# Kernel optimization log

Hardware: AMD Instinct MI355X
Metric: run time of the kernel (lower is better)

The kernel has to match this reference:

```python
import jax, jax.numpy as jnp
import numpy as np

DIM = 96
HEADS = 3
HEAD_DIM = 32
MLP_DIM = 384
WS = 4  # window size (cubic)


def _rel_indices(ws):
    # relative position indices for a ws^3 window, offset to [0, 2*ws-2]
    coords = np.stack(np.meshgrid(np.arange(ws), np.arange(ws), np.arange(ws), indexing='ij'), -1).reshape(-1, 3)
    rel = coords[:, None, :] - coords[None, :, :] + (ws - 1)  # (n, n, 3)
    return jnp.asarray(rel, dtype=jnp.int32)


def _layer_norm(x, g, b, eps=1e-5):
    m = x.mean(-1, keepdims=True)
    v = x.var(-1, keepdims=True)
    return (x - m) * jax.lax.rsqrt(v + eps) * g + b


def setup_inputs() -> dict:
    key = jax.random.key(0)
    ks = jax.random.split(key, 12)
    inner = HEADS * HEAD_DIM
    s = lambda fan_in: 1.0 / np.sqrt(fan_in)
    return {
        'x': jax.random.normal(ks[0], (2, 128, 128, 8, DIM), dtype=jnp.float32),
        'ln1_g': jnp.ones((DIM,), jnp.float32),
        'ln1_b': jnp.zeros((DIM,), jnp.float32),
        'w_qkv': jax.random.normal(ks[1], (DIM, 3 * inner), jnp.float32) * s(DIM),
        'w_out': jax.random.normal(ks[2], (inner, DIM), jnp.float32) * s(inner),
        'b_out': jnp.zeros((DIM,), jnp.float32),
        'pos_tab': jax.random.normal(ks[3], (2 * WS - 1, 2 * WS - 1, 2 * WS - 1), jnp.float32),
        'ln2_g': jnp.ones((DIM,), jnp.float32),
        'ln2_b': jnp.zeros((DIM,), jnp.float32),
        'w1': jax.random.normal(ks[4], (DIM, MLP_DIM), jnp.float32) * s(DIM),
        'b1': jnp.zeros((MLP_DIM,), jnp.float32),
        'w2': jax.random.normal(ks[5], (MLP_DIM, DIM), jnp.float32) * s(MLP_DIM),
        'b2': jnp.zeros((DIM,), jnp.float32),
    }


def reference(x, ln1_g, ln1_b, w_qkv, w_out, b_out, pos_tab, ln2_g, ln2_b, w1, b1, w2, b2):
    B, H, W, D, C = x.shape
    h, d, ws = HEADS, HEAD_DIM, WS
    nH, nW, nD = H // ws, W // ws, D // ws
    n = ws ** 3
    scale = d ** -0.5

    # --- window attention block (PreNorm + Residual) ---
    y = _layer_norm(x, ln1_g, ln1_b)
    qkv = y @ w_qkv  # (B,H,W,D,3*h*d)
    qkv = qkv.reshape(B, nH, ws, nW, ws, nD, ws, 3, h, d)
    qkv = qkv.transpose(7, 0, 8, 1, 3, 5, 2, 4, 6, 9)  # (3,B,h,nH,nW,nD,ws,ws,ws,d)
    qkv = qkv.reshape(3, B, h, nH * nW * nD, n, d)
    q, k, v = qkv[0], qkv[1], qkv[2]

    attn = jnp.einsum('bhwid,bhwjd->bhwij', q, k) * scale  # (B,h,nw,n,n)
    rel = _rel_indices(ws)
    bias = pos_tab[rel[..., 0], rel[..., 1], rel[..., 2]]  # (n,n)
    attn = jax.nn.softmax(attn + bias, axis=-1)
    o = jnp.einsum('bhwij,bhwjd->bhwid', attn, v)  # (B,h,nw,n,d)

    o = o.reshape(B, h, nH, nW, nD, ws, ws, ws, d)
    o = o.transpose(0, 2, 5, 3, 6, 4, 7, 1, 8).reshape(B, H, W, D, h * d)
    x = x + (o @ w_out + b_out)

    # --- MLP block (PreNorm + Residual), GELU exact to match nn.GELU ---
    y = _layer_norm(x, ln2_g, ln2_b)
    y = jax.nn.gelu(y @ w1 + b1, approximate=False) @ w2 + b2
    return x + y
```

## Files before the change

### kernel.cpp

```cpp
#include <hip/hip_runtime.h>

#define DIM 96
#define HEADS 3
#define HD 32
#define MLPD 384
#define NTOK 64
#define YP 104
#define QKP 200
#define VP 72
#define WSP 104
#define HP 40
#define W1P 104
#define W2P 40
#define X1P 100
#define W2PF 36
#define CH 32
#define NCH 12
#define WQT_OFF 147456
#define WOT_OFF 175104
#define WS2_NEEDED 368640

typedef unsigned short ushort_t;
typedef unsigned int uint_t;
typedef __attribute__((ext_vector_type(8))) short bf16x8;
typedef __attribute__((ext_vector_type(4))) float f32x4;

__device__ inline float b2f(ushort_t u) {
    return __uint_as_float(((uint_t)u) << 16);
}
__device__ inline ushort_t f2b(float f) {
    uint_t u = __float_as_uint(f);
    uint_t r = u + 0x7FFFu + ((u >> 16) & 1u);
    return (ushort_t)(r >> 16);
}
__device__ inline void split2(float v, ushort_t& hi, ushort_t& lo) {
    hi = f2b(v);
    float d = v - b2f(hi);
    lo = f2b(d);
}
__device__ inline void split_pack2(float v0, float v1, uint_t& hi2, uint_t& lo2) {
    uint_t u0 = __float_as_uint(v0), u1 = __float_as_uint(v1);
    hi2 = __builtin_amdgcn_perm(u1, u0, 0x07060302u);
    float d0 = v0 - __uint_as_float(u0 & 0xFFFF0000u);
    float d1 = v1 - __uint_as_float(u1 & 0xFFFF0000u);
    lo2 = __builtin_amdgcn_perm(__float_as_uint(d1), __float_as_uint(d0), 0x07060302u);
}
__device__ inline size_t grow(int bb, int wh, int ww, int wd, int t) {
    return ((size_t)((bb * 128 + wh * 4 + (t >> 4)) * 128 + ww * 4 + ((t >> 2) & 3)) * 8
            + wd * 4 + (t & 3));
}
__device__ inline float gelu_fast(float v) {
    float z = v * 0.70710678118654752f;
    float az = fabsf(z);
    float k = __frcp_rn(1.0f + 0.3275911f * az);
    float poly = k * (0.254829592f + k * (-0.284496736f + k * (1.421413741f
                 + k * (-1.453152027f + k * 1.061405429f))));
    float e = 1.0f - poly * __expf(-az * az);
    float erfv = copysignf(e, z);
    return 0.5f * v * (1.0f + erfv);
}

__global__ __launch_bounds__(256) void prep_weights(
    const float* __restrict__ w1, const float* __restrict__ w2,
    const float* __restrict__ w_qkv, const float* __restrict__ w_out,
    ushort_t* __restrict__ wt)
{
    int idx = blockIdx.x * 256 + threadIdx.x;
    if (idx >= 96 * MLPD) return;
    {
        int k = idx / MLPD, col = idx % MLPD;
        ushort_t h, l;
        split2(w1[idx], h, l);
        wt[col * 96 + k] = h;
        wt[36864 + col * 96 + k] = l;
    }
    {
        int k = idx / 96, n = idx % 96;
        int c = k >> 5, f = k & 31;
        int p = ((f & 15) >> 2) * 8 + (f >> 4) * 4 + (f & 3);
        ushort_t h, l;
        split2(w2[idx], h, l);
        wt[73728  + n * MLPD + c * 32 + p] = h;
        wt[110592 + n * MLPD + c * 32 + p] = l;
    }
    if (idx < 288 * 96) {
        int f = idx / 96, k = idx % 96;
        wt[WQT_OFF + f * 96 + k] = f2b(w_qkv[k * 288 + f]);
    }
    if (idx < 96 * 96) {
        int n = idx / 96, k = idx % 96;
        wt[WOT_OFF + n * 96 + k] = f2b(w_out[k * 96 + n]);
    }
}

__global__ __launch_bounds__(256, 3) void swin_fused_kernel(
    const float* __restrict__ x,
    const float* __restrict__ ln1_g, const float* __restrict__ ln1_b,
    const ushort_t* __restrict__ wt,
    const float* __restrict__ b_out, const float* __restrict__ pos_tab,
    const float* __restrict__ ln2_g, const float* __restrict__ ln2_b,
    const float* __restrict__ b1v, const float* __restrict__ b2v,
    float* __restrict__ out)
{
    __shared__ ushort_t ybuf[NTOK * YP];
    __shared__ ushort_t qkbuf[NTOK * QKP];
    __shared__ ushort_t vbuf[96 * VP];

    const ushort_t* wqkvt = wt + WQT_OFF;
    const ushort_t* woutt = wt + WOT_OFF;
    float* x1f = reinterpret_cast<float*>(qkbuf);

    const int tid = threadIdx.x;
    const int wv = tid >> 6;
    const int lane = tid & 63;
    const int lr = lane & 15;
    const int lk = lane >> 4;

    const int wid = blockIdx.x;
    const int wd = wid & 1;
    const int ww = (wid >> 1) & 31;
    const int wh = (wid >> 6) & 31;
    const int bb = wid >> 11;

    float breg[4][4];
    {
        const int cb = lr >> 2, cc = lr & 3;
        #pragma unroll
        for (int nt = 0; nt < 4; ++nt)
            #pragma unroll
            for (int r = 0; r < 4; ++r)
                breg[nt][r] = pos_tab[((wv - nt + 3) * 7 + (lk - cb + 3)) * 7 + (r - cc + 3)];
    }

    {
        const int t = tid >> 2, part = tid & 3;
        const float* xr = x + grow(bb, wh, ww, wd, t) * DIM + part * 24;
        float vals[24];
        #pragma unroll
        for (int i = 0; i < 6; ++i) {
            float4 v4 = *reinterpret_cast<const float4*>(xr + i * 4);
            vals[i * 4 + 0] = v4.x; vals[i * 4 + 1] = v4.y;
            vals[i * 4 + 2] = v4.z; vals[i * 4 + 3] = v4.w;
        }
        float s = 0.f, sq = 0.f;
        #pragma unroll
        for (int i = 0; i < 24; ++i) { s += vals[i]; sq += vals[i] * vals[i]; }
        s  += __shfl_xor(s, 1);  s  += __shfl_xor(s, 2);
        sq += __shfl_xor(sq, 1); sq += __shfl_xor(sq, 2);
        float mean = s * (1.f / 96.f);
        float var  = sq * (1.f / 96.f) - mean * mean;
        float rstd = rsqrtf(var + 1e-5f);
        #pragma unroll
        for (int i = 0; i < 24; i += 2) {
            int c = part * 24 + i;
            float v0 = (vals[i]     - mean) * rstd * ln1_g[c]     + ln1_b[c];
            float v1 = (vals[i + 1] - mean) * rstd * ln1_g[c + 1] + ln1_b[c + 1];
            *reinterpret_cast<uint_t*>(&ybuf[t * YP + c]) =
                (uint_t)f2b(v0) | ((uint_t)f2b(v1) << 16);
        }
    }
    asm volatile("s_waitcnt lgkmcnt(0)" ::: "memory");

    bf16x8 ay[3];
    #pragma unroll
    for (int ks = 0; ks < 3; ++ks)
        ay[ks] = *reinterpret_cast<const bf16x8*>(&ybuf[(wv * 16 + lr) * YP + ks * 32 + lk * 8]);

    #pragma unroll 3
    for (int ch = 0; ch < 9; ++ch) {
        #pragma unroll
        for (int nt = 0; nt < 2; ++nt) {
            const int feat = ch * 32 + nt * 16 + lr;
            const ushort_t* wb = &wqkvt[feat * 96 + lk * 8];
            bf16x8 b0 = *reinterpret_cast<const bf16x8*>(wb);
            bf16x8 b1 = *reinterpret_cast<const bf16x8*>(wb + 32);
            bf16x8 b2 = *reinterpret_cast<const bf16x8*>(wb + 64);
            f32x4 acc = (f32x4){0.f, 0.f, 0.f, 0.f};
            acc = __builtin_amdgcn_mfma_f32_16x16x32_bf16(ay[0], b0, acc, 0, 0, 0);
            acc = __builtin_amdgcn_mfma_f32_16x16x32_bf16(ay[1], b1, acc, 0, 0, 0);
            acc = __builtin_amdgcn_mfma_f32_16x16x32_bf16(ay[2], b2, acc, 0, 0, 0);
            if (ch < 6) {
                #pragma unroll
                for (int r = 0; r < 4; ++r)
                    qkbuf[(wv * 16 + lk * 4 + r) * QKP + feat] = f2b(acc[r]);
            } else {
                #pragma unroll
                for (int r = 0; r < 4; ++r)
                    vbuf[(feat - 192) * VP + wv * 16 + lk * 4 + r] = f2b(acc[r]);
            }
        }
    }
    __syncthreads();

    const float scale = 0.17677669529663687f;
    f32x4 oacc[6];
    #pragma unroll
    for (int i = 0; i < 6; ++i) oacc[i] = (f32x4){0.f, 0.f, 0.f, 0.f};
    ushort_t* pb = &ybuf[wv * 16 * VP];

    for (int h = 0; h < HEADS; ++h) {
        bf16x8 aq = *reinterpret_cast<const bf16x8*>(&qkbuf[(wv * 16 + lr) * QKP + h * HD + lk * 8]);
        float s[4][4];
        #pragma unroll
        for (int nt = 0; nt < 4; ++nt) {
            bf16x8 bk = *reinterpret_cast<const bf16x8*>(&qkbuf[(nt * 16 + lr) * QKP + 96 + h * HD + lk * 8]);
            f32x4 acc = (f32x4){0.f, 0.f, 0.f, 0.f};
            acc = __builtin_amdgcn_mfma_f32_16x16x32_bf16(aq, bk, acc, 0, 0, 0);
            #pragma unroll
            for (int r = 0; r < 4; ++r) s[nt][r] = acc[r] * scale + breg[nt][r];
        }
        float m[4], sum[4], inv[4];
        #pragma unroll
        for (int r = 0; r < 4; ++r) {
            m[r] = fmaxf(fmaxf(s[0][r], s[1][r]), fmaxf(s[2][r], s[3][r]));
            for (int mk = 1; mk < 16; mk <<= 1) m[r] = fmaxf(m[r], __shfl_xor(m[r], mk));
        }
        #pragma unroll
        for (int r = 0; r < 4; ++r) sum[r] = 0.f;
        #pragma unroll
        for (int nt = 0; nt < 4; ++nt)
            #pragma unroll
            for (int r = 0; r < 4; ++r) { s[nt][r] = __expf(s[nt][r] - m[r]); sum[r] += s[nt][r]; }
        #pragma unroll
        for (int r = 0; r < 4; ++r) {
            for (int mk = 1; mk < 16; mk <<= 1) sum[r] += __shfl_xor(sum[r], mk);
            inv[r] = 1.f / sum[r];
        }
        #pragma unroll
        for (int nt = 0; nt < 4; ++nt)
            #pragma unroll
            for (int r = 0; r < 4; ++r)
                pb[(lk * 4 + r) * VP + nt * 16 + lr] = f2b(s[nt][r] * inv[r]);
        asm volatile("s_waitcnt lgkmcnt(0)" ::: "memory");

        bf16x8 pa0 = *reinterpret_cast<const bf16x8*>(&pb[lr * VP + 0 * 32 + lk * 8]);
        bf16x8 pa1 = *reinterpret_cast<const bf16x8*>(&pb[lr * VP + 1 * 32 + lk * 8]);
        #pragma unroll
        for (int nt2 = 0; nt2 < 2; ++nt2) {
            f32x4 acc = oacc[h * 2 + nt2];
            bf16x8 bv0 = *reinterpret_cast<const bf16x8*>(&vbuf[(h * HD + nt2 * 16 + lr) * VP + 0 * 32 + lk * 8]);
            bf16x8 bv1 = *reinterpret_cast<const bf16x8*>(&vbuf[(h * HD + nt2 * 16 + lr) * VP + 1 * 32 + lk * 8]);
            acc = __builtin_amdgcn_mfma_f32_16x16x32_bf16(pa0, bv0, acc, 0, 0, 0);
            acc = __builtin_amdgcn_mfma_f32_16x16x32_bf16(pa1, bv1, acc, 0, 0, 0);
            oacc[h * 2 + nt2] = acc;
        }
    }
    __syncthreads();

    #pragma unroll
    for (int nt = 0; nt < 6; ++nt)
        #pragma unroll
        for (int r = 0; r < 4; ++r)
            ybuf[(wv * 16 + lk * 4 + r) * YP + nt * 16 + lr] = f2b(oacc[nt][r]);
    asm volatile("s_waitcnt lgkmcnt(0)" ::: "memory");

    bf16x8 ao[3];
    #pragma unroll
    for (int ks = 0; ks < 3; ++ks)
        ao[ks] = *reinterpret_cast<const bf16x8*>(&ybuf[(wv * 16 + lr) * YP + ks * 32 + lk * 8]);
    #pragma unroll
    for (int nt = 0; nt < 6; ++nt) {
        const ushort_t* wb = &woutt[(nt * 16 + lr) * 96 + lk * 8];
        f32x4 acc = (f32x4){0.f, 0.f, 0.f, 0.f};
        acc = __builtin_amdgcn_mfma_f32_16x16x32_bf16(ao[0], *reinterpret_cast<const bf16x8*>(wb), acc, 0, 0, 0);
        acc = __builtin_amdgcn_mfma_f32_16x16x32_bf16(ao[1], *reinterpret_cast<const bf16x8*>(wb + 32), acc, 0, 0, 0);
        acc = __builtin_amdgcn_mfma_f32_16x16x32_bf16(ao[2], *reinterpret_cast<const bf16x8*>(wb + 64), acc, 0, 0, 0);
        int col = nt * 16 + lr;
        float bias = b_out[col];
        #pragma unroll
        for (int r = 0; r < 4; ++r) {
            int t = wv * 16 + lk * 4 + r;
            x1f[t * X1P + col] = acc[r] + bias + x[grow(bb, wh, ww, wd, t) * DIM + col];
        }
    }
    asm volatile("s_waitcnt lgkmcnt(0)" ::: "memory");

    const ushort_t* gb[6];
    ushort_t* lp[6];
    #pragma unroll
    for (int i = 0; i < 6; ++i) {
        int o = tid + i * 256;
        if (i < 3) {
            int p = o / 384, rem = o % 384, r = rem / 12, j = rem % 12;
            gb[i] = wt + p * 36864 + r * 96 + j * 8;
            lp[i] = &ybuf[p * 3328 + r * 104 + j * 8];
        } else {
            int q = o - 768;
            int p = q / 384, rem = q % 384, n = rem / 4, j = rem % 4;
            gb[i] = wt + 73728 + p * 36864 + n * 384 + j * 8;
            lp[i] = &vbuf[p * 3456 + n * W2PF + j * 8];
        }
    }
    bf16x8 pf[6];
    #pragma unroll
    for (int i = 0; i < 6; ++i)
        pf[i] = *reinterpret_cast<const bf16x8*>(gb[i]);

    bf16x8 ah[3], al[3];
    {
        const int row = wv * 16 + lr;
        float v[3][8];
        float s = 0.f, sq = 0.f;
        #pragma unroll
        for (int ks = 0; ks < 3; ++ks) {
            float4 a4 = *reinterpret_cast<const float4*>(&x1f[row * X1P + ks * 32 + lk * 8]);
            float4 b4 = *reinterpret_cast<const float4*>(&x1f[row * X1P + ks * 32 + lk * 8 + 4]);
            v[ks][0] = a4.x; v[ks][1] = a4.y; v[ks][2] = a4.z; v[ks][3] = a4.w;
            v[ks][4] = b4.x; v[ks][5] = b4.y; v[ks][6] = b4.z; v[ks][7] = b4.w;
            #pragma unroll
            for (int j = 0; j < 8; ++j) { s += v[ks][j]; sq += v[ks][j] * v[ks][j]; }
        }
        s  += __shfl_xor(s, 16);  s  += __shfl_xor(s, 32);
        sq += __shfl_xor(sq, 16); sq += __shfl_xor(sq, 32);
        float mean = s * (1.f / 96.f);
        float var  = sq * (1.f / 96.f) - mean * mean;
        float rstd = rsqrtf(var + 1e-5f);
        #pragma unroll
        for (int ks = 0; ks < 3; ++ks) {
            float4 g4a = *reinterpret_cast<const float4*>(&ln2_g[ks * 32 + lk * 8]);
            float4 g4b = *reinterpret_cast<const float4*>(&ln2_g[ks * 32 + lk * 8 + 4]);
            float4 b4a = *reinterpret_cast<const float4*>(&ln2_b[ks * 32 + lk * 8]);
            float4 b4b = *reinterpret_cast<const float4*>(&ln2_b[ks * 32 + lk * 8 + 4]);
            float g[8] = {g4a.x, g4a.y, g4a.z, g4a.w, g4b.x, g4b.y, g4b.z, g4b.w};
            float bbv[8] = {b4a.x, b4a.y, b4a.z, b4a.w, b4b.x, b4b.y, b4b.z, b4b.w};
            float y[8];
            #pragma unroll
            for (int j = 0; j < 8; ++j)
                y[j] = (v[ks][j] - mean) * rstd * g[j] + bbv[j];
            union { uint4 u; bf16x8 f; } H, L;
            split_pack2(y[0], y[1], H.u.x, L.u.x);
            split_pack2(y[2], y[3], H.u.y, L.u.y);
            split_pack2(y[4], y[5], H.u.z, L.u.z);
            split_pack2(y[6], y[7], H.u.w, L.u.w);
            ah[ks] = H.f;
            al[ks] = L.f;
        }
    }

    f32x4 macc[6];
    #pragma unroll
    for (int nt = 0; nt < 6; ++nt) macc[nt] = (f32x4){0.f, 0.f, 0.f, 0.f};

    for (int c = 0; c < NCH; ++c) {
        __syncthreads();
        #pragma unroll
        for (int i = 0; i < 6; ++i)
            *reinterpret_cast<bf16x8*>(lp[i]) = pf[i];
        if (c + 1 < NCH) {
            const int coff1 = (c + 1) * 3072, coff2 = (c + 1) * 32;
            #pragma unroll
            for (int i = 0; i < 3; ++i)
                pf[i] = *reinterpret_cast<const bf16x8*>(gb[i] + coff1);
            #pragma unroll
            for (int i = 3; i < 6; ++i)
                pf[i] = *reinterpret_cast<const bf16x8*>(gb[i] + coff2);
        }
        __syncthreads();

        f32x4 hpre[2];
        #pragma unroll
        for (int nt = 0; nt < 2; ++nt) {
            const int roff = (nt * 16 + lr) * 104 + lk * 8;
            bf16x8 wh0 = *reinterpret_cast<const bf16x8*>(&ybuf[roff]);
            bf16x8 wh1 = *reinterpret_cast<const bf16x8*>(&ybuf[roff + 32]);
            bf16x8 wh2 = *reinterpret_cast<const bf16x8*>(&ybuf[roff + 64]);
            bf16x8 wl0 = *reinterpret_cast<const bf16x8*>(&ybuf[3328 + roff]);
            bf16x8 wl1 = *reinterpret_cast<const bf16x8*>(&ybuf[3328 + roff + 32]);
            bf16x8 wl2 = *reinterpret_cast<const bf16x8*>(&ybuf[3328 + roff + 64]);
            f32x4 acc = (f32x4){0.f, 0.f, 0.f, 0.f};
            acc = __builtin_amdgcn_mfma_f32_16x16x32_bf16(wh0, ah[0], acc, 0, 0, 0);
            acc = __builtin_amdgcn_mfma_f32_16x16x32_bf16(wh0, al[0], acc, 0, 0, 0);
            acc = __builtin_amdgcn_mfma_f32_16x16x32_bf16(wl0, ah[0], acc, 0, 0, 0);
            acc = __builtin_amdgcn_mfma_f32_16x16x32_bf16(wh1, ah[1], acc, 0, 0, 0);
            acc = __builtin_amdgcn_mfma_f32_16x16x32_bf16(wh1, al[1], acc, 0, 0, 0);
            acc = __builtin_amdgcn_mfma_f32_16x16x32_bf16(wl1, ah[1], acc, 0, 0, 0);
            acc = __builtin_amdgcn_mfma_f32_16x16x32_bf16(wh2, ah[2], acc, 0, 0, 0);
            acc = __builtin_amdgcn_mfma_f32_16x16x32_bf16(wh2, al[2], acc, 0, 0, 0);
            acc = __builtin_amdgcn_mfma_f32_16x16x32_bf16(wl2, ah[2], acc, 0, 0, 0);
            hpre[nt] = acc;
        }

        float4 b40 = *reinterpret_cast<const float4*>(&b1v[c * CH + 0 * 16 + lk * 4]);
        float4 b41 = *reinterpret_cast<const float4*>(&b1v[c * CH + 1 * 16 + lk * 4]);
        bf16x8 a2h, a2l;
        {
            float g0 = gelu_fast(hpre[0][0] + b40.x);
            float g1 = gelu_fast(hpre[0][1] + b40.y);
            float g2 = gelu_fast(hpre[0][2] + b40.z);
            float g3 = gelu_fast(hpre[0][3] + b40.w);
            float g4 = gelu_fast(hpre[1][0] + b41.x);
            float g5 = gelu_fast(hpre[1][1] + b41.y);
            float g6 = gelu_fast(hpre[1][2] + b41.z);
            float g7 = gelu_fast(hpre[1][3] + b41.w);
            union { uint4 u; bf16x8 f; } H, L;
            split_pack2(g0, g1, H.u.x, L.u.x);
            split_pack2(g2, g3, H.u.y, L.u.y);
            split_pack2(g4, g5, H.u.z, L.u.z);
            split_pack2(g6, g7, H.u.w, L.u.w);
            a2h = H.f;
            a2l = L.f;
        }

        #pragma unroll
        for (int nt2 = 0; nt2 < 6; ++nt2) {
            const int noff = (nt2 * 16 + lr) * W2PF + lk * 8;
            bf16x8 wh = *reinterpret_cast<const bf16x8*>(&vbuf[noff]);
            bf16x8 wl = *reinterpret_cast<const bf16x8*>(&vbuf[3456 + noff]);
            f32x4 acc = macc[nt2];
            acc = __builtin_amdgcn_mfma_f32_16x16x32_bf16(a2h, wh, acc, 0, 0, 0);
            acc = __builtin_amdgcn_mfma_f32_16x16x32_bf16(a2h, wl, acc, 0, 0, 0);
            acc = __builtin_amdgcn_mfma_f32_16x16x32_bf16(a2l, wh, acc, 0, 0, 0);
            macc[nt2] = acc;
        }
    }

    #pragma unroll
    for (int nt = 0; nt < 6; ++nt) {
        int col = nt * 16 + lr;
        float bias = b2v[col];
        #pragma unroll
        for (int r = 0; r < 4; ++r) {
            int t = wv * 16 + lk * 4 + r;
            out[grow(bb, wh, ww, wd, t) * DIM + col] =
                macc[nt][r] + bias + x1f[t * X1P + col];
        }
    }
}

__global__ __launch_bounds__(256) void attn_mfma_kernel(
    const float* __restrict__ x,
    const float* __restrict__ ln1_g, const float* __restrict__ ln1_b,
    const float* __restrict__ w_qkv,
    const float* __restrict__ w_out, const float* __restrict__ b_out,
    const float* __restrict__ pos_tab,
    float* __restrict__ out)
{
    __shared__ ushort_t ybuf[NTOK * YP];
    __shared__ ushort_t qkbuf[NTOK * QKP];
    __shared__ ushort_t vbuf[96 * VP];
    __shared__ ushort_t wstage[CH * WSP];
    __shared__ float pos[343];

    const int tid = threadIdx.x;
    const int wv = tid >> 6;
    const int lane = tid & 63;
    const int lr = lane & 15;
    const int lk = lane >> 4;

    const int wid = blockIdx.x;
    const int wd = wid & 1;
    const int ww = (wid >> 1) & 31;
    const int wh = (wid >> 6) & 31;
    const int bb = wid >> 11;

    for (int e = tid; e < 343; e += 256) pos[e] = pos_tab[e];

    {
        const int t = tid >> 2, part = tid & 3;
        const float* xr = x + grow(bb, wh, ww, wd, t) * DIM + part * 24;
        float vals[24];
        for (int i = 0; i < 6; ++i) {
            float4 v4 = *reinterpret_cast<const float4*>(xr + i * 4);
            vals[i * 4 + 0] = v4.x; vals[i * 4 + 1] = v4.y;
            vals[i * 4 + 2] = v4.z; vals[i * 4 + 3] = v4.w;
        }
        float s = 0.f, sq = 0.f;
        for (int i = 0; i < 24; ++i) { s += vals[i]; sq += vals[i] * vals[i]; }
        s  += __shfl_xor(s, 1);  s  += __shfl_xor(s, 2);
        sq += __shfl_xor(sq, 1); sq += __shfl_xor(sq, 2);
        float mean = s * (1.f / 96.f);
        float var  = sq * (1.f / 96.f) - mean * mean;
        float rstd = rsqrtf(var + 1e-5f);
        for (int i = 0; i < 24; i += 2) {
            int c = part * 24 + i;
            float v0 = (vals[i]     - mean) * rstd * ln1_g[c]     + ln1_b[c];
            float v1 = (vals[i + 1] - mean) * rstd * ln1_g[c + 1] + ln1_b[c + 1];
            *reinterpret_cast<uint_t*>(&ybuf[t * YP + c]) =
                (uint_t)f2b(v0) | ((uint_t)f2b(v1) << 16);
        }
    }
    __syncthreads();

    bf16x8 ay[3];
    for (int ks = 0; ks < 3; ++ks)
        ay[ks] = *reinterpret_cast<const bf16x8*>(&ybuf[(wv * 16 + lr) * YP + ks * 32 + lk * 8]);

    for (int ch = 0; ch < 9; ++ch) {
        for (int e = tid; e < 32 * 48; e += 256) {
            int n = e & 31, kp = e >> 5;
            float a = w_qkv[(2 * kp) * 288 + ch * 32 + n];
            float b = w_qkv[(2 * kp + 1) * 288 + ch * 32 + n];
            *reinterpret_cast<uint_t*>(&wstage[n * WSP + 2 * kp]) =
                (uint_t)f2b(a) | ((uint_t)f2b(b) << 16);
        }
        __syncthreads();

        for (int nt = 0; nt < 2; ++nt) {
            f32x4 acc = (f32x4){0.f, 0.f, 0.f, 0.f};
            for (int ks = 0; ks < 3; ++ks) {
                bf16x8 bf = *reinterpret_cast<const bf16x8*>(&wstage[(nt * 16 + lr) * WSP + ks * 32 + lk * 8]);
                acc = __builtin_amdgcn_mfma_f32_16x16x32_bf16(ay[ks], bf, acc, 0, 0, 0);
            }
            int feat = ch * 32 + nt * 16 + lr;
            if (ch < 6) {
                for (int r = 0; r < 4; ++r)
                    qkbuf[(wv * 16 + lk * 4 + r) * QKP + feat] = f2b(acc[r]);
            } else {
                for (int r = 0; r < 4; ++r)
                    vbuf[(feat - 192) * VP + wv * 16 + lk * 4 + r] = f2b(acc[r]);
            }
        }
        __syncthreads();
    }

    float breg[4][4];
    {
        const int cb = lr >> 2, cc = lr & 3;
        for (int nt = 0; nt < 4; ++nt)
            for (int r = 0; r < 4; ++r)
                breg[nt][r] = pos[((wv - nt + 3) * 7 + (lk - cb + 3)) * 7 + (r - cc + 3)];
    }

    const float scale = 0.17677669529663687f;
    f32x4 oacc[6];
    for (int i = 0; i < 6; ++i) oacc[i] = (f32x4){0.f, 0.f, 0.f, 0.f};
    ushort_t* pb = &ybuf[wv * 16 * VP];

    for (int h = 0; h < HEADS; ++h) {
        bf16x8 aq = *reinterpret_cast<const bf16x8*>(&qkbuf[(wv * 16 + lr) * QKP + h * HD + lk * 8]);
        float s[4][4];
        for (int nt = 0; nt < 4; ++nt) {
            bf16x8 bk = *reinterpret_cast<const bf16x8*>(&qkbuf[(nt * 16 + lr) * QKP + 96 + h * HD + lk * 8]);
            f32x4 acc = (f32x4){0.f, 0.f, 0.f, 0.f};
            acc = __builtin_amdgcn_mfma_f32_16x16x32_bf16(aq, bk, acc, 0, 0, 0);
            for (int r = 0; r < 4; ++r) s[nt][r] = acc[r] * scale + breg[nt][r];
        }
        float m[4], sum[4], inv[4];
        for (int r = 0; r < 4; ++r) {
            m[r] = fmaxf(fmaxf(s[0][r], s[1][r]), fmaxf(s[2][r], s[3][r]));
            for (int mk = 1; mk < 16; mk <<= 1) m[r] = fmaxf(m[r], __shfl_xor(m[r], mk));
        }
        for (int r = 0; r < 4; ++r) sum[r] = 0.f;
        for (int nt = 0; nt < 4; ++nt)
            for (int r = 0; r < 4; ++r) { s[nt][r] = __expf(s[nt][r] - m[r]); sum[r] += s[nt][r]; }
        for (int r = 0; r < 4; ++r) {
            for (int mk = 1; mk < 16; mk <<= 1) sum[r] += __shfl_xor(sum[r], mk);
            inv[r] = 1.f / sum[r];
        }
        for (int nt = 0; nt < 4; ++nt)
            for (int r = 0; r < 4; ++r)
                pb[(lk * 4 + r) * VP + nt * 16 + lr] = f2b(s[nt][r] * inv[r]);
        asm volatile("s_waitcnt lgkmcnt(0)" ::: "memory");

        bf16x8 pa0 = *reinterpret_cast<const bf16x8*>(&pb[lr * VP + 0 * 32 + lk * 8]);
        bf16x8 pa1 = *reinterpret_cast<const bf16x8*>(&pb[lr * VP + 1 * 32 + lk * 8]);
        for (int nt2 = 0; nt2 < 2; ++nt2) {
            f32x4 acc = oacc[h * 2 + nt2];
            bf16x8 bv0 = *reinterpret_cast<const bf16x8*>(&vbuf[(h * HD + nt2 * 16 + lr) * VP + 0 * 32 + lk * 8]);
            bf16x8 bv1 = *reinterpret_cast<const bf16x8*>(&vbuf[(h * HD + nt2 * 16 + lr) * VP + 1 * 32 + lk * 8]);
            acc = __builtin_amdgcn_mfma_f32_16x16x32_bf16(pa0, bv0, acc, 0, 0, 0);
            acc = __builtin_amdgcn_mfma_f32_16x16x32_bf16(pa1, bv1, acc, 0, 0, 0);
            oacc[h * 2 + nt2] = acc;
        }
    }
    __syncthreads();

    for (int nt = 0; nt < 6; ++nt)
        for (int r = 0; r < 4; ++r)
            ybuf[(wv * 16 + lk * 4 + r) * YP + nt * 16 + lr] = f2b(oacc[nt][r]);
    for (int e = tid; e < 96 * 48; e += 256) {
        int n = e % 96, kp = e / 96;
        float a = w_out[(2 * kp) * 96 + n];
        float b = w_out[(2 * kp + 1) * 96 + n];
        *reinterpret_cast<uint_t*>(&qkbuf[n * WSP + 2 * kp]) =
            (uint_t)f2b(a) | ((uint_t)f2b(b) << 16);
    }
    __syncthreads();

    bf16x8 ao[3];
    for (int ks = 0; ks < 3; ++ks)
        ao[ks] = *reinterpret_cast<const bf16x8*>(&ybuf[(wv * 16 + lr) * YP + ks * 32 + lk * 8]);
    for (int nt = 0; nt < 6; ++nt) {
        f32x4 acc = (f32x4){0.f, 0.f, 0.f, 0.f};
        for (int ks = 0; ks < 3; ++ks) {
            bf16x8 bw = *reinterpret_cast<const bf16x8*>(&qkbuf[(nt * 16 + lr) * WSP + ks * 32 + lk * 8]);
            acc = __builtin_amdgcn_mfma_f32_16x16x32_bf16(ao[ks], bw, acc, 0, 0, 0);
        }
        int col = nt * 16 + lr;
        float bias = b_out[col];
        for (int r = 0; r < 4; ++r) {
            int t = wv * 16 + lk * 4 + r;
            size_t g = grow(bb, wh, ww, wd, t);
            out[g * DIM + col] = acc[r] + bias + x[g * DIM + col];
        }
    }
}

__global__ __launch_bounds__(256) void mlp_stage_kernel(
    float* __restrict__ io,
    const float* __restrict__ ln2_g, const float* __restrict__ ln2_b,
    const float* __restrict__ w1, const float* __restrict__ b1v,
    const float* __restrict__ w2, const float* __restrict__ b2v)
{
    __shared__ ushort_t yhi[NTOK * YP], ylo[NTOK * YP];
    __shared__ ushort_t hhi[NTOK * HP], hlo[NTOK * HP];
    __shared__ ushort_t whi[96 * HP],  wlo[96 * HP];

    const int tid = threadIdx.x;
    const int wv = tid >> 6;
    const int lane = tid & 63;
    const int lr = lane & 15;
    const int lk = lane >> 4;
    const size_t base = (size_t)blockIdx.x * NTOK * DIM;

    {
        const int t = tid >> 2, part = tid & 3;
        const float* xr = io + base + t * DIM + part * 24;
        float vals[24];
        for (int i = 0; i < 6; ++i) {
            float4 v4 = *reinterpret_cast<const float4*>(xr + i * 4);
            vals[i * 4 + 0] = v4.x; vals[i * 4 + 1] = v4.y;
            vals[i * 4 + 2] = v4.z; vals[i * 4 + 3] = v4.w;
        }
        float s = 0.f, sq = 0.f;
        for (int i = 0; i < 24; ++i) { s += vals[i]; sq += vals[i] * vals[i]; }
        s  += __shfl_xor(s, 1);  s  += __shfl_xor(s, 2);
        sq += __shfl_xor(sq, 1); sq += __shfl_xor(sq, 2);
        float mean = s * (1.f / 96.f);
        float var  = sq * (1.f / 96.f) - mean * mean;
        float rstd = rsqrtf(var + 1e-5f);
        for (int i = 0; i < 24; i += 2) {
            int c = part * 24 + i;
            float v0 = (vals[i]     - mean) * rstd * ln2_g[c]     + ln2_b[c];
            float v1 = (vals[i + 1] - mean) * rstd * ln2_g[c + 1] + ln2_b[c + 1];
            ushort_t h0, l0, h1, l1;
            split2(v0, h0, l0); split2(v1, h1, l1);
            *reinterpret_cast<uint_t*>(&yhi[t * YP + c]) = (uint_t)h0 | ((uint_t)h1 << 16);
            *reinterpret_cast<uint_t*>(&ylo[t * YP + c]) = (uint_t)l0 | ((uint_t)l1 << 16);
        }
    }

    f32x4 oacc[6];
    for (int nt = 0; nt < 6; ++nt) oacc[nt] = (f32x4){0.f, 0.f, 0.f, 0.f};

    for (int c = 0; c < NCH; ++c) {
        for (int idx = tid; idx < CH * 96; idx += 256) {
            int col = idx & 31, k = idx >> 5;
            ushort_t h, l;
            split2(w1[k * MLPD + c * CH + col], h, l);
            whi[col * W1P + k] = h;
            wlo[col * W1P + k] = l;
        }
        __syncthreads();

        bf16x8 ah[3], al[3];
        for (int ks = 0; ks < 3; ++ks) {
            ah[ks] = *reinterpret_cast<const bf16x8*>(&yhi[(wv * 16 + lr) * YP + ks * 32 + lk * 8]);
            al[ks] = *reinterpret_cast<const bf16x8*>(&ylo[(wv * 16 + lr) * YP + ks * 32 + lk * 8]);
        }
        for (int nt = 0; nt < 2; ++nt) {
            f32x4 acc = (f32x4){0.f, 0.f, 0.f, 0.f};
            for (int ks = 0; ks < 3; ++ks) {
                bf16x8 bh = *reinterpret_cast<const bf16x8*>(&whi[(nt * 16 + lr) * W1P + ks * 32 + lk * 8]);
                bf16x8 bl = *reinterpret_cast<const bf16x8*>(&wlo[(nt * 16 + lr) * W1P + ks * 32 + lk * 8]);
                acc = __builtin_amdgcn_mfma_f32_16x16x32_bf16(ah[ks], bh, acc, 0, 0, 0);
                acc = __builtin_amdgcn_mfma_f32_16x16x32_bf16(ah[ks], bl, acc, 0, 0, 0);
                acc = __builtin_amdgcn_mfma_f32_16x16x32_bf16(al[ks], bh, acc, 0, 0, 0);
            }
            float bias = b1v[c * CH + nt * 16 + lr];
            for (int r = 0; r < 4; ++r) {
                float ge = gelu_fast(acc[r] + bias);
                ushort_t h, l;
                split2(ge, h, l);
                hhi[(wv * 16 + lk * 4 + r) * HP + nt * 16 + lr] = h;
                hlo[(wv * 16 + lk * 4 + r) * HP + nt * 16 + lr] = l;
            }
        }
        __syncthreads();

        for (int idx = tid; idx < 96 * CH; idx += 256) {
            int n = idx % 96, k = idx / 96;
            ushort_t h, l;
            split2(w2[(c * CH + k) * DIM + n], h, l);
            whi[n * W2P + k] = h;
            wlo[n * W2P + k] = l;
        }
        __syncthreads();

        bf16x8 a2h = *reinterpret_cast<const bf16x8*>(&hhi[(wv * 16 + lr) * HP + lk * 8]);
        bf16x8 a2l = *reinterpret_cast<const bf16x8*>(&hlo[(wv * 16 + lr) * HP + lk * 8]);
        for (int nt = 0; nt < 6; ++nt) {
            f32x4 acc = oacc[nt];
            bf16x8 bh = *reinterpret_cast<const bf16x8*>(&whi[(nt * 16 + lr) * W2P + lk * 8]);
            bf16x8 bl = *reinterpret_cast<const bf16x8*>(&wlo[(nt * 16 + lr) * W2P + lk * 8]);
            acc = __builtin_amdgcn_mfma_f32_16x16x32_bf16(a2h, bh, acc, 0, 0, 0);
            acc = __builtin_amdgcn_mfma_f32_16x16x32_bf16(a2h, bl, acc, 0, 0, 0);
            acc = __builtin_amdgcn_mfma_f32_16x16x32_bf16(a2l, bh, acc, 0, 0, 0);
            oacc[nt] = acc;
        }
        __syncthreads();
    }

    for (int nt = 0; nt < 6; ++nt) {
        float bias = b2v[nt * 16 + lr];
        for (int r = 0; r < 4; ++r) {
            size_t gi = base + (size_t)(wv * 16 + lk * 4 + r) * DIM + nt * 16 + lr;
            io[gi] = oacc[nt][r] + bias + io[gi];
        }
    }
}

extern "C" void kernel_launch(void* const* d_in, const int* in_sizes, int n_in,
                              void* d_out, int out_size, void* d_ws, size_t ws_size,
                              hipStream_t stream) {
    const float* x      = (const float*)d_in[0];
    const float* ln1_g  = (const float*)d_in[1];
    const float* ln1_b  = (const float*)d_in[2];
    const float* w_qkv  = (const float*)d_in[3];
    const float* w_out  = (const float*)d_in[4];
    const float* b_out  = (const float*)d_in[5];
    const float* pos    = (const float*)d_in[6];
    const float* ln2_g  = (const float*)d_in[7];
    const float* ln2_b  = (const float*)d_in[8];
    const float* w1     = (const float*)d_in[9];
    const float* b1v    = (const float*)d_in[10];
    const float* w2     = (const float*)d_in[11];
    const float* b2v    = (const float*)d_in[12];
    float* out = (float*)d_out;

    if (ws_size >= (size_t)WS2_NEEDED) {
        ushort_t* wt = (ushort_t*)d_ws;
        prep_weights<<<(96 * MLPD + 255) / 256, 256, 0, stream>>>(w1, w2, w_qkv, w_out, wt);
        swin_fused_kernel<<<4096, 256, 0, stream>>>(
            x, ln1_g, ln1_b, wt, b_out, pos, ln2_g, ln2_b, b1v, b2v, out);
    } else {
        attn_mfma_kernel<<<4096, 256, 0, stream>>>(
            x, ln1_g, ln1_b, w_qkv, w_out, b_out, pos, out);
        mlp_stage_kernel<<<4096, 256, 0, stream>>>(out, ln2_g, ln2_b, w1, b1v, w2, b2v);
    }
}
```

Measured before the change: 292.4 us.

## Shrink shared memory and read MLP weights straight from global for 4 blocks/CU

Repacks LDS into one smaller buffer: Q is written into the LN output buffer and K gets its own narrower buffer, with x1 aliased onto K. The per-chunk staging of W1/W2 through LDS, with its two barriers per chunk and register prefetch, is removed, so the MLP MFMAs load weight fragments directly from global memory (expected to hit L2/L1). Launch bounds rise from 3 to 4 blocks per CU to use the freed LDS and registers. The trade is more global/cache traffic and exposed load latency in the MLP loop in exchange for higher occupancy and no syncs.

```diff
diff --git a/kernel.cpp b/kernel.cpp
--- a/kernel.cpp
+++ b/kernel.cpp
@@ -6,6 +6,7 @@
 #define MLPD 384
 #define NTOK 64
 #define YP 104
+#define KP 104
 #define QKP 200
 #define VP 72
 #define WSP 104
@@ -13,7 +14,6 @@
 #define W1P 104
 #define W2P 40
 #define X1P 100
-#define W2PF 36
 #define CH 32
 #define NCH 12
 #define WQT_OFF 147456
@@ -93,7 +93,7 @@
     }
 }
 
-__global__ __launch_bounds__(256, 3) void swin_fused_kernel(
+__global__ __launch_bounds__(256, 4) void swin_fused_kernel(
     const float* __restrict__ x,
     const float* __restrict__ ln1_g, const float* __restrict__ ln1_b,
     const ushort_t* __restrict__ wt,
@@ -102,13 +102,14 @@
     const float* __restrict__ b1v, const float* __restrict__ b2v,
     float* __restrict__ out)
 {
-    __shared__ ushort_t ybuf[NTOK * YP];
-    __shared__ ushort_t qkbuf[NTOK * QKP];
-    __shared__ ushort_t vbuf[96 * VP];
+    __shared__ __align__(16) ushort_t smem[20224];
+    ushort_t* ybuf = smem;
+    ushort_t* kbuf = smem + 6656;
+    ushort_t* vbuf = smem + 13312;
+    float* x1f = reinterpret_cast<float*>(smem + 6656);
 
     const ushort_t* wqkvt = wt + WQT_OFF;
     const ushort_t* woutt = wt + WOT_OFF;
-    float* x1f = reinterpret_cast<float*>(qkbuf);
 
     const int tid = threadIdx.x;
     const int wv = tid >> 6;
@@ -179,10 +180,14 @@
             acc = __builtin_amdgcn_mfma_f32_16x16x32_bf16(ay[0], b0, acc, 0, 0, 0);
             acc = __builtin_amdgcn_mfma_f32_16x16x32_bf16(ay[1], b1, acc, 0, 0, 0);
             acc = __builtin_amdgcn_mfma_f32_16x16x32_bf16(ay[2], b2, acc, 0, 0, 0);
-            if (ch < 6) {
+            if (ch < 3) {
                 #pragma unroll
                 for (int r = 0; r < 4; ++r)
-                    qkbuf[(wv * 16 + lk * 4 + r) * QKP + feat] = f2b(acc[r]);
+                    ybuf[(wv * 16 + lk * 4 + r) * YP + feat] = f2b(acc[r]);
+            } else if (ch < 6) {
+                #pragma unroll
+                for (int r = 0; r < 4; ++r)
+                    kbuf[(wv * 16 + lk * 4 + r) * KP + (feat - 96)] = f2b(acc[r]);
             } else {
                 #pragma unroll
                 for (int r = 0; r < 4; ++r)
@@ -192,20 +197,26 @@
     }
     __syncthreads();
 
+    bf16x8 aq[3];
+    #pragma unroll
+    for (int h = 0; h < HEADS; ++h)
+        aq[h] = *reinterpret_cast<const bf16x8*>(&ybuf[(wv * 16 + lr) * YP + h * HD + lk * 8]);
+    asm volatile("s_waitcnt lgkmcnt(0)" ::: "memory");
+
     const float scale = 0.17677669529663687f;
     f32x4 oacc[6];
     #pragma unroll
     for (int i = 0; i < 6; ++i) oacc[i] = (f32x4){0.f, 0.f, 0.f, 0.f};
-    ushort_t* pb = &ybuf[wv * 16 * VP];
-
+    ushort_t* pb = &ybuf[wv * 16 * YP];
+
+    #pragma unroll
     for (int h = 0; h < HEADS; ++h) {
-        bf16x8 aq = *reinterpret_cast<const bf16x8*>(&qkbuf[(wv * 16 + lr) * QKP + h * HD + lk * 8]);
         float s[4][4];
         #pragma unroll
         for (int nt = 0; nt < 4; ++nt) {
-            bf16x8 bk = *reinterpret_cast<const bf16x8*>(&qkbuf[(nt * 16 + lr) * QKP + 96 + h * HD + lk * 8]);
+            bf16x8 bk = *reinterpret_cast<const bf16x8*>(&kbuf[(nt * 16 + lr) * KP + h * HD + lk * 8]);
             f32x4 acc = (f32x4){0.f, 0.f, 0.f, 0.f};
-            acc = __builtin_amdgcn_mfma_f32_16x16x32_bf16(aq, bk, acc, 0, 0, 0);
+            acc = __builtin_amdgcn_mfma_f32_16x16x32_bf16(aq[h], bk, acc, 0, 0, 0);
             #pragma unroll
             for (int r = 0; r < 4; ++r) s[nt][r] = acc[r] * scale + breg[nt][r];
         }
@@ -274,27 +285,6 @@
         }
     }
     asm volatile("s_waitcnt lgkmcnt(0)" ::: "memory");
-
-    const ushort_t* gb[6];
-    ushort_t* lp[6];
-    #pragma unroll
-    for (int i = 0; i < 6; ++i) {
-        int o = tid + i * 256;
-        if (i < 3) {
-            int p = o / 384, rem = o % 384, r = rem / 12, j = rem % 12;
-            gb[i] = wt + p * 36864 + r * 96 + j * 8;
-            lp[i] = &ybuf[p * 3328 + r * 104 + j * 8];
-        } else {
-            int q = o - 768;
-            int p = q / 384, rem = q % 384, n = rem / 4, j = rem % 4;
-            gb[i] = wt + 73728 + p * 36864 + n * 384 + j * 8;
-            lp[i] = &vbuf[p * 3456 + n * W2PF + j * 8];
-        }
-    }
-    bf16x8 pf[6];
-    #pragma unroll
-    for (int i = 0; i < 6; ++i)
-        pf[i] = *reinterpret_cast<const bf16x8*>(gb[i]);
 
     bf16x8 ah[3], al[3];
     {
@@ -341,32 +331,22 @@
     #pragma unroll
     for (int nt = 0; nt < 6; ++nt) macc[nt] = (f32x4){0.f, 0.f, 0.f, 0.f};
 
+    const ushort_t* w1p = wt + lr * 96 + lk * 8;
+    const ushort_t* w2p = wt + 73728 + lr * MLPD + lk * 8;
+
     for (int c = 0; c < NCH; ++c) {
-        __syncthreads();
-        #pragma unroll
-        for (int i = 0; i < 6; ++i)
-            *reinterpret_cast<bf16x8*>(lp[i]) = pf[i];
-        if (c + 1 < NCH) {
-            const int coff1 = (c + 1) * 3072, coff2 = (c + 1) * 32;
-            #pragma unroll
-            for (int i = 0; i < 3; ++i)
-                pf[i] = *reinterpret_cast<const bf16x8*>(gb[i] + coff1);
-            #pragma unroll
-            for (int i = 3; i < 6; ++i)
-                pf[i] = *reinterpret_cast<const bf16x8*>(gb[i] + coff2);
-        }
-        __syncthreads();
+        const int co1 = c * 3072, co2 = c * 32;
 
         f32x4 hpre[2];
         #pragma unroll
         for (int nt = 0; nt < 2; ++nt) {
-            const int roff = (nt * 16 + lr) * 104 + lk * 8;
-            bf16x8 wh0 = *reinterpret_cast<const bf16x8*>(&ybuf[roff]);
-            bf16x8 wh1 = *reinterpret_cast<const bf16x8*>(&ybuf[roff + 32]);
-            bf16x8 wh2 = *reinterpret_cast<const bf16x8*>(&ybuf[roff + 64]);
-            bf16x8 wl0 = *reinterpret_cast<const bf16x8*>(&ybuf[3328 + roff]);
-            bf16x8 wl1 = *reinterpret_cast<const bf16x8*>(&ybuf[3328 + roff + 32]);
-            bf16x8 wl2 = *reinterpret_cast<const bf16x8*>(&ybuf[3328 + roff + 64]);
+            const ushort_t* wb = w1p + co1 + nt * 1536;
+            bf16x8 wh0 = *reinterpret_cast<const bf16x8*>(wb);
+            bf16x8 wh1 = *reinterpret_cast<const bf16x8*>(wb + 32);
+            bf16x8 wh2 = *reinterpret_cast<const bf16x8*>(wb + 64);
+            bf16x8 wl0 = *reinterpret_cast<const bf16x8*>(wb + 36864);
+            bf16x8 wl1 = *reinterpret_cast<const bf16x8*>(wb + 36864 + 32);
+            bf16x8 wl2 = *reinterpret_cast<const bf16x8*>(wb + 36864 + 64);
             f32x4 acc = (f32x4){0.f, 0.f, 0.f, 0.f};
             acc = __builtin_amdgcn_mfma_f32_16x16x32_bf16(wh0, ah[0], acc, 0, 0, 0);
             acc = __builtin_amdgcn_mfma_f32_16x16x32_bf16(wh0, al[0], acc, 0, 0, 0);
@@ -403,9 +383,9 @@
 
         #pragma unroll
         for (int nt2 = 0; nt2 < 6; ++nt2) {
-            const int noff = (nt2 * 16 + lr) * W2PF + lk * 8;
-            bf16x8 wh = *reinterpret_cast<const bf16x8*>(&vbuf[noff]);
-            bf16x8 wl = *reinterpret_cast<const bf16x8*>(&vbuf[3456 + noff]);
+            const ushort_t* wb2 = w2p + co2 + nt2 * 6144;
+            bf16x8 wh = *reinterpret_cast<const bf16x8*>(wb2);
+            bf16x8 wl = *reinterpret_cast<const bf16x8*>(wb2 + 36864);
             f32x4 acc = macc[nt2];
             acc = __builtin_amdgcn_mfma_f32_16x16x32_bf16(a2h, wh, acc, 0, 0, 0);
             acc = __builtin_amdgcn_mfma_f32_16x16x32_bf16(a2h, wl, acc, 0, 0, 0);
```

Measured after the change: 494.6 us. 1.69x slower.
